# Performance work log

Hardware: AMD Instinct MI355X
Metric: run time of the kernel (lower is better)

## Reference

```python
import jax, jax.numpy as jnp
import numpy as np

DIM = 1024
N_HEADS = 16
HEAD_DIM = DIM // N_HEADS


def setup_inputs() -> dict:
    key = jax.random.key(0)
    k_x, k_wqkv, k_bqkv, k_wp, k_bp = jax.random.split(key, 5)
    s = 1.0 / np.sqrt(DIM)
    return {
        "x": jax.random.normal(k_x, (2, 2048, DIM), dtype=jnp.float32),
        "w_qkv": jax.random.uniform(k_wqkv, (3 * DIM, DIM), minval=-s, maxval=s, dtype=jnp.float32),
        "b_qkv": jax.random.uniform(k_bqkv, (3 * DIM,), minval=-s, maxval=s, dtype=jnp.float32),
        "w_proj": jax.random.uniform(k_wp, (DIM, DIM), minval=-s, maxval=s, dtype=jnp.float32),
        "b_proj": jax.random.uniform(k_bp, (DIM,), minval=-s, maxval=s, dtype=jnp.float32),
    }


def reference(x, w_qkv, b_qkv, w_proj, b_proj):
    B, S, D = x.shape
    H, Hd = N_HEADS, HEAD_DIM
    scale = jnp.asarray(Hd, x.dtype) ** 0.5
    qkv = x @ w_qkv.T + b_qkv                      # [B, S, 3D]
    q, k, v = jnp.split(qkv, 3, axis=-1)
    # [B, S, D] -> [B, H, S, Hd]
    q = q.reshape(B, S, H, Hd).transpose(0, 2, 1, 3)
    k = k.reshape(B, S, H, Hd).transpose(0, 2, 1, 3)
    v = v.reshape(B, S, H, Hd).transpose(0, 2, 1, 3)
    attn = jnp.einsum("bhqd,bhkd->bhqk", q, k) / scale
    attn = jax.nn.softmax(attn, axis=-1)
    out = jnp.einsum("bhqk,bhkd->bhqd", attn, v)   # [B, H, S, Hd]
    out = out.transpose(0, 2, 1, 3).reshape(B, S, D)
    return out @ w_proj.T + b_proj
```

## Files before the change

kernel.cpp:

```cpp
#include <hip/hip_runtime.h>

typedef __bf16 bf16;
typedef __bf16 bf16x4 __attribute__((ext_vector_type(4)));
typedef __bf16 bf16x8 __attribute__((ext_vector_type(8)));
typedef float f32x4 __attribute__((ext_vector_type(4)));
typedef float f32x16 __attribute__((ext_vector_type(16)));

#define DIMD 1024
#define NHEAD 16
#define HDIM 64
#define BATCH 2
#define SEQ 2048
#define MTOT (BATCH*SEQ)

#define OFF_VT    (0ull)
#define OFF_WQKV  (8ull<<20)
#define OFF_OB    (8ull<<20)
#define OFF_WPROJ (0ull)

__device__ __forceinline__ void g2l16(const void* g, void* l) {
  __builtin_amdgcn_global_load_lds(
      (const __attribute__((address_space(1))) void*)g,
      (__attribute__((address_space(3))) void*)l,
      16, 0, 0);
}

__global__ __launch_bounds__(256) void cvt_kernel(const float* __restrict__ in,
                                                  bf16* __restrict__ out, int n4) {
  int i = blockIdx.x * blockDim.x + threadIdx.x;
  if (i < n4) {
    float4 v = ((const float4*)in)[i];
    bf16x4 o = { (bf16)v.x, (bf16)v.y, (bf16)v.z, (bf16)v.w };
    ((bf16x4*)out)[i] = o;
  }
}

__global__ __launch_bounds__(256, 2) void gemm_qkv(
    const float* __restrict__ x, const bf16* __restrict__ Wt,
    const float* __restrict__ bias,
    bf16* __restrict__ Qb, bf16* __restrict__ Kb, bf16* __restrict__ Vt)
{
  __shared__ bf16 lA[128 * 32];
  __shared__ bf16 lB[128 * 32];
  const int tid = threadIdx.x;
  const int wave = tid >> 6, lane = tid & 63;
  const int l15 = lane & 15, quad = lane >> 4;
  const int wm = wave >> 1, wn = wave & 1;
  const int tm = blockIdx.y * 128, tn = blockIdx.x * 128;

  f32x4 acc[4][4] = {};

  const int arowA = tid >> 1;
  const int acolA = (tid & 1) * 16;
  const int brow = tid >> 2;
  const int bchunk = (tid & 3) * 8;

  for (int kb = 0; kb < DIMD; kb += 32) {
    const float* gx = &x[(size_t)(tm + arowA) * DIMD + kb + acolA];
    float4 v0 = ((const float4*)gx)[0];
    float4 v1 = ((const float4*)gx)[1];
    float4 v2 = ((const float4*)gx)[2];
    float4 v3 = ((const float4*)gx)[3];
    __syncthreads();
    const bf16* gB = &Wt[(size_t)(tn + brow) * DIMD + kb + bchunk];
    g2l16(gB,                     &lB[wave * 512]);
    g2l16(gB + (size_t)64 * DIMD, &lB[2048 + wave * 512]);
    bf16x8 a0 = { (bf16)v0.x, (bf16)v0.y, (bf16)v0.z, (bf16)v0.w,
                  (bf16)v1.x, (bf16)v1.y, (bf16)v1.z, (bf16)v1.w };
    bf16x8 a1 = { (bf16)v2.x, (bf16)v2.y, (bf16)v2.z, (bf16)v2.w,
                  (bf16)v3.x, (bf16)v3.y, (bf16)v3.z, (bf16)v3.w };
    *(bf16x8*)&lA[arowA * 32 + acolA]     = a0;
    *(bf16x8*)&lA[arowA * 32 + acolA + 8] = a1;
    __syncthreads();

    bf16x8 af[4], bfr[4];
#pragma unroll
    for (int i = 0; i < 4; i++)
      af[i] = *(const bf16x8*)&lA[(wm * 64 + i * 16 + l15) * 32 + quad * 8];
#pragma unroll
    for (int i = 0; i < 4; i++)
      bfr[i] = *(const bf16x8*)&lB[(wn * 64 + i * 16 + l15) * 32 + quad * 8];
#pragma unroll
    for (int i = 0; i < 4; i++)
#pragma unroll
      for (int j = 0; j < 4; j++)
        acc[i][j] = __builtin_amdgcn_mfma_f32_16x16x32_bf16(af[i], bfr[j], acc[i][j], 0, 0, 0);
  }

  const int sel = tn >> 10;
#pragma unroll
  for (int j = 0; j < 4; j++) {
    const int n = tn + wn * 64 + j * 16 + l15;
    const float bv = bias[n];
    const int d = n & 1023, h = d >> 6, hd = d & 63;
#pragma unroll
    for (int i = 0; i < 4; i++) {
      const int mbase = tm + wm * 64 + i * 16 + quad * 4;
#pragma unroll
      for (int r = 0; r < 4; r++) {
        const int mm = mbase + r;
        const int b = mm >> 11, s = mm & 2047;
        const int bh = b * NHEAD + h;
        float v = acc[i][j][r] + bv;
        if (sel == 0)      Qb[((size_t)bh * SEQ + s) * HDIM + hd] = (bf16)(v * 0.125f);
        else if (sel == 1) Kb[((size_t)bh * SEQ + s) * HDIM + hd] = (bf16)v;
        else               Vt[((size_t)bh * HDIM + hd) * SEQ + s] = (bf16)v;
      }
    }
  }
}

__global__ __launch_bounds__(256, 2) void gemm_proj(
    const bf16* __restrict__ A, const bf16* __restrict__ Bt,
    const float* __restrict__ bias, float* __restrict__ out)
{
  __shared__ bf16 lA[64 * 32];
  __shared__ bf16 lB[128 * 32];
  const int tid = threadIdx.x;
  const int wave = tid >> 6, lane = tid & 63;
  const int l15 = lane & 15, quad = lane >> 4;
  const int tm = blockIdx.y * 64, tn = blockIdx.x * 128;

  f32x4 acc[4][2] = {};
  const int row = tid >> 2;
  const int ch = (tid & 3) * 8;

  for (int kb = 0; kb < DIMD; kb += 32) {
    __syncthreads();
    g2l16(&A[(size_t)(tm + row) * DIMD + kb + ch],        &lA[wave * 512]);
    g2l16(&Bt[(size_t)(tn + row) * DIMD + kb + ch],       &lB[wave * 512]);
    g2l16(&Bt[(size_t)(tn + 64 + row) * DIMD + kb + ch],  &lB[2048 + wave * 512]);
    __syncthreads();

    bf16x8 af[4], bfr[2];
#pragma unroll
    for (int i = 0; i < 4; i++)
      af[i] = *(const bf16x8*)&lA[(i * 16 + l15) * 32 + quad * 8];
#pragma unroll
    for (int j = 0; j < 2; j++)
      bfr[j] = *(const bf16x8*)&lB[(wave * 32 + j * 16 + l15) * 32 + quad * 8];
#pragma unroll
    for (int i = 0; i < 4; i++)
#pragma unroll
      for (int j = 0; j < 2; j++)
        acc[i][j] = __builtin_amdgcn_mfma_f32_16x16x32_bf16(af[i], bfr[j], acc[i][j], 0, 0, 0);
  }

#pragma unroll
  for (int j = 0; j < 2; j++) {
    const int n = tn + wave * 32 + j * 16 + l15;
    const float bv = bias[n];
#pragma unroll
    for (int i = 0; i < 4; i++) {
      const int mbase = tm + i * 16 + quad * 4;
#pragma unroll
      for (int r = 0; r < 4; r++)
        out[(size_t)(mbase + r) * DIMD + n] = acc[i][j][r] + bv;
    }
  }
}

#define LSTR 72
__global__ __launch_bounds__(256, 2) void attn_kernel(
    const bf16* __restrict__ Qb, const bf16* __restrict__ Kb,
    const bf16* __restrict__ Vt, bf16* __restrict__ Ob)
{
  __shared__ bf16 lK[64 * LSTR];
  __shared__ bf16 lV[64 * LSTR];
  __shared__ bf16 lP[4][32 * LSTR];

  const int tid = threadIdx.x;
  const int wave = tid >> 6, lane = tid & 63;
  const int l31 = lane & 31, h = lane >> 5;
  const int qt = blockIdx.x & 15;
  const int bh = blockIdx.x >> 4;

  const int qrow = qt * 128 + wave * 32 + l31;
  const bf16* qp = Qb + ((size_t)bh * SEQ + qrow) * HDIM + h * 8;
  bf16x8 qf[4];
#pragma unroll
  for (int c = 0; c < 4; c++) qf[c] = *(const bf16x8*)(qp + c * 16);

  f32x16 o0 = {}, o1 = {};
  float mrow = -1e30f, lrow = 0.f;

  for (int kt = 0; kt < SEQ / 64; kt++) {
    __syncthreads();
#pragma unroll
    for (int it = 0; it < 2; it++) {
      const int idx = tid + it * 256;
      const int row = idx >> 3, ch = (idx & 7) * 8;
      *(uint4*)&lK[row * LSTR + ch] =
          *(const uint4*)&Kb[((size_t)bh * SEQ + kt * 64 + row) * HDIM + ch];
      *(uint4*)&lV[row * LSTR + ch] =
          *(const uint4*)&Vt[((size_t)bh * HDIM + row) * SEQ + kt * 64 + ch];
    }
    __syncthreads();

    f32x16 s0 = {}, s1 = {};
#pragma unroll
    for (int c = 0; c < 4; c++) {
      bf16x8 k0 = *(const bf16x8*)&lK[l31 * LSTR + c * 16 + h * 8];
      bf16x8 k1 = *(const bf16x8*)&lK[(32 + l31) * LSTR + c * 16 + h * 8];
      s0 = __builtin_amdgcn_mfma_f32_32x32x16_bf16(k0, qf[c], s0, 0, 0, 0);
      s1 = __builtin_amdgcn_mfma_f32_32x32x16_bf16(k1, qf[c], s1, 0, 0, 0);
    }

    float mx = -1e30f;
#pragma unroll
    for (int r = 0; r < 16; r++) { mx = fmaxf(mx, s0[r]); mx = fmaxf(mx, s1[r]); }
    mx = fmaxf(mx, __shfl_xor(mx, 32, 64));
    const float nm = fmaxf(mrow, mx);
    const float alpha = __expf(mrow - nm);
    mrow = nm;

    float rs = 0.f;
#pragma unroll
    for (int r = 0; r < 16; r++) {
      const float p0 = __expf(s0[r] - nm);
      const float p1 = __expf(s1[r] - nm);
      s0[r] = p0; s1[r] = p1;
      rs += p0 + p1;
    }
    rs += __shfl_xor(rs, 32, 64);
    lrow = lrow * alpha + rs;
#pragma unroll
    for (int r = 0; r < 16; r++) { o0[r] *= alpha; o1[r] *= alpha; }

#pragma unroll
    for (int g = 0; g < 4; g++) {
      bf16x4 pa = { (bf16)s0[4*g], (bf16)s0[4*g+1], (bf16)s0[4*g+2], (bf16)s0[4*g+3] };
      bf16x4 pb = { (bf16)s1[4*g], (bf16)s1[4*g+1], (bf16)s1[4*g+2], (bf16)s1[4*g+3] };
      *(bf16x4*)&lP[wave][l31 * LSTR + g * 8 + h * 4]      = pa;
      *(bf16x4*)&lP[wave][l31 * LSTR + 32 + g * 8 + h * 4] = pb;
    }
    bf16x8 pf[4];
#pragma unroll
    for (int c = 0; c < 4; c++)
      pf[c] = *(const bf16x8*)&lP[wave][l31 * LSTR + c * 16 + h * 8];

#pragma unroll
    for (int c = 0; c < 4; c++) {
      bf16x8 v0 = *(const bf16x8*)&lV[l31 * LSTR + c * 16 + h * 8];
      bf16x8 v1 = *(const bf16x8*)&lV[(32 + l31) * LSTR + c * 16 + h * 8];
      o0 = __builtin_amdgcn_mfma_f32_32x32x16_bf16(v0, pf[c], o0, 0, 0, 0);
      o1 = __builtin_amdgcn_mfma_f32_32x32x16_bf16(v1, pf[c], o1, 0, 0, 0);
    }
  }

  const int b = bh >> 4, head = bh & 15;
  const float inv = 1.f / lrow;
  const size_t base = ((size_t)b * SEQ + qrow) * DIMD + head * HDIM;
#pragma unroll
  for (int g = 0; g < 4; g++) {
    bf16x4 oa = { (bf16)(o0[4*g] * inv), (bf16)(o0[4*g+1] * inv),
                  (bf16)(o0[4*g+2] * inv), (bf16)(o0[4*g+3] * inv) };
    bf16x4 ob = { (bf16)(o1[4*g] * inv), (bf16)(o1[4*g+1] * inv),
                  (bf16)(o1[4*g+2] * inv), (bf16)(o1[4*g+3] * inv) };
    *(bf16x4*)&Ob[base + g * 8 + h * 4]      = oa;
    *(bf16x4*)&Ob[base + 32 + g * 8 + h * 4] = ob;
  }
}

extern "C" void kernel_launch(void* const* d_in, const int* in_sizes, int n_in,
                              void* d_out, int out_size, void* d_ws, size_t ws_size,
                              hipStream_t stream) {
  const float* x      = (const float*)d_in[0];
  const float* w_qkv  = (const float*)d_in[1];
  const float* b_qkv  = (const float*)d_in[2];
  const float* w_proj = (const float*)d_in[3];
  const float* b_proj = (const float*)d_in[4];
  float* out = (float*)d_out;
  char* ws = (char*)d_ws;

  bf16* Qb = (bf16*)d_out;
  bf16* Kb = (bf16*)d_out + (size_t)MTOT * DIMD;
  bf16* Vt     = (bf16*)(ws + OFF_VT);
  bf16* wqkvb  = (bf16*)(ws + OFF_WQKV);
  bf16* Ob     = (bf16*)(ws + OFF_OB);
  bf16* wprojb = (bf16*)(ws + OFF_WPROJ);

  cvt_kernel<<<(3 * DIMD * DIMD / 4) / 256, 256, 0, stream>>>(w_qkv, wqkvb, 3 * DIMD * DIMD / 4);
  gemm_qkv<<<dim3(24, 32), 256, 0, stream>>>(x, wqkvb, b_qkv, Qb, Kb, Vt);
  attn_kernel<<<BATCH * NHEAD * (SEQ / 128), 256, 0, stream>>>(Qb, Kb, Vt, Ob);
  cvt_kernel<<<(DIMD * DIMD / 4) / 256, 256, 0, stream>>>(w_proj, wprojb, DIMD * DIMD / 4);
  gemm_proj<<<dim3(8, 64), 256, 0, stream>>>(Ob, wprojb, b_proj, out);
}
```

Baseline: 222.5 us.

## Double-buffer K/V tiles via register prefetch, use exp2 softmax, vectorize V stores

```diff
diff --git a/kernel.cpp b/kernel.cpp
--- a/kernel.cpp
+++ b/kernel.cpp
@@ -12,6 +12,8 @@
 #define BATCH 2
 #define SEQ 2048
 #define MTOT (BATCH*SEQ)
+
+#define EXP2F(x) __builtin_amdgcn_exp2f(x)
 
 #define OFF_VT    (0ull)
 #define OFF_WQKV  (8ull<<20)
@@ -96,15 +98,21 @@
 #pragma unroll
     for (int i = 0; i < 4; i++) {
       const int mbase = tm + wm * 64 + i * 16 + quad * 4;
-#pragma unroll
-      for (int r = 0; r < 4; r++) {
-        const int mm = mbase + r;
-        const int b = mm >> 11, s = mm & 2047;
-        const int bh = b * NHEAD + h;
-        float v = acc[i][j][r] + bv;
-        if (sel == 0)      Qb[((size_t)bh * SEQ + s) * HDIM + hd] = (bf16)(v * 0.125f);
-        else if (sel == 1) Kb[((size_t)bh * SEQ + s) * HDIM + hd] = (bf16)v;
-        else               Vt[((size_t)bh * HDIM + hd) * SEQ + s] = (bf16)v;
+      const int b = mbase >> 11, s0 = mbase & 2047;
+      const int bh = b * NHEAD + h;
+      if (sel == 2) {
+        bf16x4 vv = { (bf16)(acc[i][j][0] + bv), (bf16)(acc[i][j][1] + bv),
+                      (bf16)(acc[i][j][2] + bv), (bf16)(acc[i][j][3] + bv) };
+        *(bf16x4*)&Vt[((size_t)bh * HDIM + hd) * SEQ + s0] = vv;
+      } else {
+#pragma unroll
+        for (int r = 0; r < 4; r++) {
+          float v = acc[i][j][r] + bv;
+          if (sel == 0)
+            Qb[((size_t)bh * SEQ + s0 + r) * HDIM + hd] = (bf16)(v * 0.18033688f);
+          else
+            Kb[((size_t)bh * SEQ + s0 + r) * HDIM + hd] = (bf16)v;
+        }
       }
     }
   }
@@ -165,15 +173,15 @@
     const bf16* __restrict__ Qb, const bf16* __restrict__ Kb,
     const bf16* __restrict__ Vt, bf16* __restrict__ Ob)
 {
-  __shared__ bf16 lK[64 * LSTR];
-  __shared__ bf16 lV[64 * LSTR];
+  __shared__ bf16 lKV[2][2][64 * LSTR];
   __shared__ bf16 lP[4][32 * LSTR];
 
   const int tid = threadIdx.x;
   const int wave = tid >> 6, lane = tid & 63;
   const int l31 = lane & 31, h = lane >> 5;
-  const int qt = blockIdx.x & 15;
-  const int bh = blockIdx.x >> 4;
+  const int xcd = blockIdx.x & 7, grp = blockIdx.x >> 3;
+  const int bh = xcd + 8 * (grp & 3);
+  const int qt = grp >> 2;
 
   const int qrow = qt * 128 + wave * 32 + l31;
   const bf16* qp = Qb + ((size_t)bh * SEQ + qrow) * HDIM + h * 8;
@@ -181,27 +189,39 @@
 #pragma unroll
   for (int c = 0; c < 4; c++) qf[c] = *(const bf16x8*)(qp + c * 16);
 
+  const int srow = tid >> 3;
+  const int sch = (tid & 7) * 8;
+  const bf16* kg = Kb + ((size_t)bh * SEQ + srow) * HDIM + sch;
+  const bf16* vg = Vt + ((size_t)bh * HDIM + srow) * SEQ + sch;
+
+  uint4 kr0 = *(const uint4*)(kg);
+  uint4 kr1 = *(const uint4*)(kg + 32 * HDIM);
+  uint4 vr0 = *(const uint4*)(vg);
+  uint4 vr1 = *(const uint4*)(vg + 32 * SEQ);
+
   f32x16 o0 = {}, o1 = {};
   float mrow = -1e30f, lrow = 0.f;
 
   for (int kt = 0; kt < SEQ / 64; kt++) {
-    __syncthreads();
-#pragma unroll
-    for (int it = 0; it < 2; it++) {
-      const int idx = tid + it * 256;
-      const int row = idx >> 3, ch = (idx & 7) * 8;
-      *(uint4*)&lK[row * LSTR + ch] =
-          *(const uint4*)&Kb[((size_t)bh * SEQ + kt * 64 + row) * HDIM + ch];
-      *(uint4*)&lV[row * LSTR + ch] =
-          *(const uint4*)&Vt[((size_t)bh * HDIM + row) * SEQ + kt * 64 + ch];
-    }
-    __syncthreads();
+    bf16* sK = lKV[kt & 1][0];
+    bf16* sV = lKV[kt & 1][1];
+    *(uint4*)&sK[srow * LSTR + sch]        = kr0;
+    *(uint4*)&sK[(32 + srow) * LSTR + sch] = kr1;
+    *(uint4*)&sV[srow * LSTR + sch]        = vr0;
+    *(uint4*)&sV[(32 + srow) * LSTR + sch] = vr1;
+    __syncthreads();
+
+    const int ktn = (kt + 1) & (SEQ / 64 - 1);
+    kr0 = *(const uint4*)(kg + (size_t)ktn * 64 * HDIM);
+    kr1 = *(const uint4*)(kg + (size_t)ktn * 64 * HDIM + 32 * HDIM);
+    vr0 = *(const uint4*)(vg + ktn * 64);
+    vr1 = *(const uint4*)(vg + ktn * 64 + 32 * SEQ);
 
     f32x16 s0 = {}, s1 = {};
 #pragma unroll
     for (int c = 0; c < 4; c++) {
-      bf16x8 k0 = *(const bf16x8*)&lK[l31 * LSTR + c * 16 + h * 8];
-      bf16x8 k1 = *(const bf16x8*)&lK[(32 + l31) * LSTR + c * 16 + h * 8];
+      bf16x8 k0 = *(const bf16x8*)&sK[l31 * LSTR + c * 16 + h * 8];
+      bf16x8 k1 = *(const bf16x8*)&sK[(32 + l31) * LSTR + c * 16 + h * 8];
       s0 = __builtin_amdgcn_mfma_f32_32x32x16_bf16(k0, qf[c], s0, 0, 0, 0);
       s1 = __builtin_amdgcn_mfma_f32_32x32x16_bf16(k1, qf[c], s1, 0, 0, 0);
     }
@@ -211,14 +231,14 @@
     for (int r = 0; r < 16; r++) { mx = fmaxf(mx, s0[r]); mx = fmaxf(mx, s1[r]); }
     mx = fmaxf(mx, __shfl_xor(mx, 32, 64));
     const float nm = fmaxf(mrow, mx);
-    const float alpha = __expf(mrow - nm);
+    const float alpha = EXP2F(mrow - nm);
     mrow = nm;
 
     float rs = 0.f;
 #pragma unroll
     for (int r = 0; r < 16; r++) {
-      const float p0 = __expf(s0[r] - nm);
-      const float p1 = __expf(s1[r] - nm);
+      const float p0 = EXP2F(s0[r] - nm);
+      const float p1 = EXP2F(s1[r] - nm);
       s0[r] = p0; s1[r] = p1;
       rs += p0 + p1;
     }
@@ -241,8 +261,8 @@
 
 #pragma unroll
     for (int c = 0; c < 4; c++) {
-      bf16x8 v0 = *(const bf16x8*)&lV[l31 * LSTR + c * 16 + h * 8];
-      bf16x8 v1 = *(const bf16x8*)&lV[(32 + l31) * LSTR + c * 16 + h * 8];
+      bf16x8 v0 = *(const bf16x8*)&sV[l31 * LSTR + c * 16 + h * 8];
+      bf16x8 v1 = *(const bf16x8*)&sV[(32 + l31) * LSTR + c * 16 + h * 8];
       o0 = __builtin_amdgcn_mfma_f32_32x32x16_bf16(v0, pf[c], o0, 0, 0, 0);
       o1 = __builtin_amdgcn_mfma_f32_32x32x16_bf16(v1, pf[c], o1, 0, 0, 0);
     }
```

New measurement: 204.9 us. -8.0%, faster.
